# Optimization experiments

Hardware: AMD Instinct MI355X
Metric: run time of the kernel (lower is better)

## Reference

```python
import math
import jax, jax.numpy as jnp
import numpy as np

B, N, D, NC, TMAX = 8, 4096, 1024, 512, 1000


def setup_inputs() -> dict:
    key = jax.random.key(0)
    ks = jax.random.split(key, 12)
    tokens = jax.random.normal(ks[0], (B, N, D), jnp.float32)
    ctx_C = jax.random.normal(ks[1], (B, NC, D), jnp.float32)
    t = jax.random.randint(ks[2], (B,), 0, TMAX, dtype=jnp.int32)
    rare_mask = jax.random.bernoulli(ks[3], 0.05, (B, N))
    # Linear params stored as (in, out); scaled so scores straddle 0.5
    ctx_w = jax.random.normal(ks[4], (D, D // 4), jnp.float32) / math.sqrt(D)
    ctx_b = jax.random.normal(ks[5], (D // 4,), jnp.float32) * 0.01
    t_proj_w = jax.random.normal(ks[6], (D, D), jnp.float32) / math.sqrt(D)
    t_proj_b = jax.random.normal(ks[7], (D,), jnp.float32) * 0.01
    HIN = D + D // 4 + D  # 2304
    w1 = jax.random.normal(ks[8], (HIN, D // 2), jnp.float32) / math.sqrt(HIN)
    b1 = jax.random.normal(ks[9], (D // 2,), jnp.float32) * 0.01
    w2 = jax.random.normal(ks[10], (D // 2,), jnp.float32) * 0.1
    b2 = jnp.zeros((1,), jnp.float32)
    return {"tokens": tokens, "ctx_C": ctx_C, "t": t, "rare_mask": rare_mask,
            "ctx_w": ctx_w, "ctx_b": ctx_b, "t_proj_w": t_proj_w,
            "t_proj_b": t_proj_b, "w1": w1, "b1": b1, "w2": w2, "b2": b2}


def reference(tokens, ctx_C, t, rare_mask, ctx_w, ctx_b, t_proj_w, t_proj_b, w1, b1, w2, b2):
    Bb, Nn, Dd = tokens.shape
    half = Dd // 2
    # sinusoidal timestep embedding buffer (matches torch register_buffer)
    freq = jnp.exp(-math.log(10000.0) * jnp.arange(half, dtype=jnp.float32) / max(half - 1, 1))
    # bottlenecked context: mean over ctx tokens -> (B, D//4)
    ctx_bn = ctx_C.mean(axis=1) @ ctx_w + ctx_b
    args = t.astype(jnp.float32)[:, None] * freq[None, :]            # (B, half)
    emb = jnp.concatenate([jnp.sin(args), jnp.cos(args)], axis=-1)   # (B, D)
    t_emb = emb @ t_proj_w + t_proj_b                                # (B, D)
    x = jnp.concatenate([
        tokens,
        jnp.broadcast_to(ctx_bn[:, None, :], (Bb, Nn, Dd // 4)),
        jnp.broadcast_to(t_emb[:, None, :], (Bb, Nn, Dd)),
    ], axis=-1)                                                       # (B, N, 2.25D)
    h = jax.nn.relu(x @ w1 + b1)                                      # (B, N, D//2)
    scores = jax.nn.sigmoid(h @ w2 + b2)                              # (B, N)
    skip = (scores > 0.5) & jnp.logical_not(rare_mask)
    min_active = max(1, int(Nn * 0.2))
    active = jnp.logical_not(skip).sum(axis=-1)                       # (B,)
    deficit = jnp.maximum(min_active - active, 0)                     # (B,)
    masked = jnp.where(skip, scores, jnp.inf)
    rank = jnp.argsort(jnp.argsort(masked, axis=-1), axis=-1)         # rank among skipped, ascending score
    skip = skip & jnp.logical_not(rank < deficit[:, None])
    return skip, scores
```

## Files before the change

### kernel.cpp

```cpp
#include <hip/hip_runtime.h>
#include <math.h>

#define NN 4096
#define DD 1024
#define M_TOT 32768
#define H1 512
#define MIN_ACTIVE 819
#define MARGIN 0.03f
#define MAXFIX 8192

typedef __bf16 bf16x8 __attribute__((ext_vector_type(8)));
typedef float f32x4 __attribute__((ext_vector_type(4)));

__device__ __forceinline__ unsigned short f2bf(float f) {
    unsigned int u = __float_as_uint(f);
    return (unsigned short)((u + 0x7FFFu + ((u >> 16) & 1u)) >> 16);
}

__device__ __forceinline__ void glds16(const unsigned short* g, unsigned short* l) {
    __builtin_amdgcn_global_load_lds(
        (const __attribute__((address_space(1))) unsigned int*)g,
        (__attribute__((address_space(3))) unsigned int*)l, 16, 0, 0);
}

__global__ void convB_pmean_kernel(const float* __restrict__ w1, unsigned short* __restrict__ w1tt,
                                   const float* __restrict__ ctx, float* __restrict__ pmean,
                                   const unsigned char* __restrict__ rare, int* __restrict__ mode,
                                   int* __restrict__ fixcnt) {
    __shared__ float tile[32][65];
    __shared__ int nonbin, oneoff;
    int blk = blockIdx.x;
    int tid = threadIdx.x;
    if (blk < 256) {
        int t = blk >> 3;
        int c0 = (blk & 7) * 64;
        #pragma unroll
        for (int i = 0; i < 8; ++i) {
            int idx = tid + 256 * i;
            int kk = idx >> 6, cc = idx & 63;
            tile[kk][cc] = w1[(size_t)(t * 32 + kk) * H1 + c0 + cc];
        }
        __syncthreads();
        {
            int cc = tid >> 2, jp = tid & 3;
            int c = c0 + cc;
            int j = jp ^ ((c >> 1) & 3);
            unsigned int w[4];
            #pragma unroll
            for (int q = 0; q < 4; ++q)
                w[q] = (unsigned int)f2bf(tile[j * 8 + 2 * q][cc])
                     | ((unsigned int)f2bf(tile[j * 8 + 2 * q + 1][cc]) << 16);
            uint4 v; v.x = w[0]; v.y = w[1]; v.z = w[2]; v.w = w[3];
            *(uint4*)(w1tt + ((size_t)t * 512 + c) * 32 + jp * 8) = v;
        }
        if (blk == 0) {
            if (tid == 0) { nonbin = 0; oneoff = 0; *fixcnt = 0; }
            __syncthreads();
            int lnon = 0, lone = 0;
            for (int i = tid; i < 32768; i += 256) {
                unsigned char b = rare[i];
                if (b > 1) lnon = 1;
                else if (b == 1 && (i & 3) != 0) lone = 1;
            }
            if (lnon) atomicOr(&nonbin, 1);
            if (lone) atomicOr(&oneoff, 1);
            __syncthreads();
            if (tid == 0) *mode = nonbin ? 2 : (oneoff ? 1 : 0);
        }
    } else {
        int pblk = blk - 256;
        int b = pblk >> 5, dq = (pblk >> 3) & 3, nz = pblk & 7;
        int d = dq * 256 + tid;
        const float* base = ctx + ((size_t)(b * 512 + nz * 64)) * DD + d;
        float acc = 0.f;
        for (int n = 0; n < 64; ++n) acc += base[(size_t)n * DD];
        pmean[(b * 8 + nz) * DD + d] = acc;
    }
}

__global__ __launch_bounds__(256) void midk_kernel(
    const float* __restrict__ pmean, const int* __restrict__ t,
    const float* __restrict__ ctx_w, const float* __restrict__ ctx_b,
    const float* __restrict__ tpw, const float* __restrict__ tpb,
    float* __restrict__ ctx_bn, float* __restrict__ t_emb) {
    __shared__ float sh[1024];
    __shared__ float red8[8][32];
    __shared__ float red4[4][64];
    int tid = threadIdx.x;
    if (blockIdx.x < 64) {
        int b = blockIdx.x >> 3, cg = blockIdx.x & 7;
        for (int j = tid; j < 1024; j += 256) {
            float s = 0.f;
            #pragma unroll
            for (int nz = 0; nz < 8; ++nz) s += pmean[(b * 8 + nz) * DD + j];
            sh[j] = s * (1.f / 512.f);
        }
        __syncthreads();
        int c = cg * 32 + (tid & 31), ks = tid >> 5;
        const float* mb = sh + ks * 128;
        const float* wb = ctx_w + (size_t)(ks * 128) * 256 + c;
        float acc = 0.f;
        for (int i = 0; i < 128; ++i) acc += mb[i] * wb[(size_t)i * 256];
        red8[ks][tid & 31] = acc;
        __syncthreads();
        if (tid < 32) {
            float s = 0.f;
            for (int k = 0; k < 8; ++k) s += red8[k][tid];
            ctx_bn[b * 256 + cg * 32 + tid] = s + ctx_b[cg * 32 + tid];
        }
    } else {
        int blk = blockIdx.x - 64;
        int b = blk >> 4, cg = blk & 15;
        double tv = (double)t[b];
        const double neg_ln = -log(10000.0) / 511.0;
        for (int j = tid; j < 1024; j += 256) {
            int jj = j & 511;
            double arg = tv * exp(neg_ln * (double)jj);
            sh[j] = (float)((j < 512) ? sin(arg) : cos(arg));
        }
        __syncthreads();
        int c = cg * 64 + (tid & 63), ks = tid >> 6;
        const float* eb = sh + ks * 256;
        const float* wb = tpw + (size_t)(ks * 256) * DD + c;
        float acc = 0.f;
        for (int i = 0; i < 256; ++i) acc += eb[i] * wb[(size_t)i * DD];
        red4[ks][tid & 63] = acc;
        __syncthreads();
        if (tid < 64) {
            float s = red4[0][tid] + red4[1][tid] + red4[2][tid] + red4[3][tid];
            t_emb[b * DD + cg * 64 + tid] = s + tpb[cg * 64 + tid];
        }
    }
}

__global__ void baseh_kernel(const float* __restrict__ ctx_bn, const float* __restrict__ t_emb,
                             const float* __restrict__ w1, const float* __restrict__ b1,
                             float* __restrict__ base_h) {
    __shared__ float red[8][32];
    int b = blockIdx.x, cg = blockIdx.y;
    int c = cg * 32 + (threadIdx.x & 31), ks = threadIdx.x >> 5;
    float acc = 0.f;
    for (int i = 0; i < 160; ++i) {
        int k = ks * 160 + i;
        float v = (k < 256) ? ctx_bn[b * 256 + k] : t_emb[b * DD + k - 256];
        acc += v * w1[(size_t)(1024 + k) * H1 + c];
    }
    red[ks][threadIdx.x & 31] = acc;
    __syncthreads();
    if (threadIdx.x < 32) {
        float s = 0.f;
        for (int k = 0; k < 8; ++k) s += red[k][threadIdx.x];
        base_h[b * H1 + cg * 32 + threadIdx.x] = s + b1[cg * 32 + threadIdx.x];
    }
}

__global__ __launch_bounds__(512, 2) void gemm_kernel(
    const float* __restrict__ tokens, const unsigned short* __restrict__ w1tt,
    const float* __restrict__ baseh, const float* __restrict__ w2,
    const float* __restrict__ b2, const void* __restrict__ rare,
    const int* __restrict__ mode_p, float* __restrict__ out,
    int* __restrict__ fixcnt, int* __restrict__ fixlist) {
    __shared__ unsigned short As[2][128 * 40];
    __shared__ unsigned short Bs[3][512 * 32];
    __shared__ float red[128][4];
    int tid = threadIdx.x;
    int lane = tid & 63, wid = tid >> 6;
    int wm = wid >> 2, wn = wid & 3;
    int la = lane & 15, lk = lane >> 4;
    int row0 = blockIdx.x * 128;

    f32x4 acc[4][8];
    #pragma unroll
    for (int i = 0; i < 4; ++i)
        #pragma unroll
        for (int j = 0; j < 8; ++j)
            acc[i][j] = (f32x4){0.f, 0.f, 0.f, 0.f};

    float4 sa0[2], sa1[2];
    #define LOAD_A(kt_, S_) { \
        _Pragma("unroll") \
        for (int i = 0; i < 2; ++i) { \
            int id = tid + 512 * i; \
            int r = id >> 3, xk = id & 7; \
            S_[i] = *(const float4*)(tokens + (size_t)(row0 + r) * DD + (kt_) + xk * 4); \
        } }
    #define WRITE_A(bb_, S_) { \
        _Pragma("unroll") \
        for (int i = 0; i < 2; ++i) { \
            int id = tid + 512 * i; \
            int r = id >> 3, xk = id & 7; \
            ushort4 h; \
            h.x = f2bf(S_[i].x); h.y = f2bf(S_[i].y); \
            h.z = f2bf(S_[i].z); h.w = f2bf(S_[i].w); \
            *(ushort4*)(&As[bb_][r * 40 + xk * 4]) = h; \
        } }
    #define STAGE_B(t_, bb_) { \
        const unsigned short* gsrc = w1tt + (size_t)(t_) * 512 * 32; \
        _Pragma("unroll") \
        for (int q = 0; q < 4; ++q) { \
            int chunk = wid * 4 + q; \
            glds16(gsrc + chunk * 512 + lane * 8, &Bs[bb_][chunk * 512]); \
        } }

    LOAD_A(0, sa0);
    STAGE_B(0, 0);
    STAGE_B(1, 1);
    WRITE_A(0, sa0);
    LOAD_A(32, sa1);
    __builtin_amdgcn_sched_barrier(0);
    asm volatile("s_waitcnt vmcnt(6)" ::: "memory");
    asm volatile("s_waitcnt lgkmcnt(0)" ::: "memory");
    __builtin_amdgcn_s_barrier();
    __builtin_amdgcn_sched_barrier(0);

    for (int t = 0; t < 32; ++t) {
        int bb = t & 1;
        const unsigned short* bsrc = Bs[t % 3];
        bf16x8 af[4], bfr[8];
        #pragma unroll
        for (int mf = 0; mf < 4; ++mf) {
            int r = wm * 64 + mf * 16 + la;
            af[mf] = *(const bf16x8*)(&As[bb][r * 40 + lk * 8]);
        }
        #pragma unroll
        for (int nf = 0; nf < 8; ++nf) {
            int c = wn * 128 + nf * 16 + la;
            int sw = lk ^ ((c >> 1) & 3);
            bfr[nf] = *(const bf16x8*)(&bsrc[c * 32 + sw * 8]);
        }
        __builtin_amdgcn_s_setprio(1);
        #pragma unroll
        for (int mf = 0; mf < 4; ++mf)
            #pragma unroll
            for (int nf = 0; nf < 8; ++nf)
                acc[mf][nf] = __builtin_amdgcn_mfma_f32_16x16x32_bf16(af[mf], bfr[nf], acc[mf][nf], 0, 0, 0);
        __builtin_amdgcn_s_setprio(0);
        __builtin_amdgcn_sched_barrier(0);
        if (t < 31) {
            if (t & 1) { WRITE_A(bb ^ 1, sa0) } else { WRITE_A(bb ^ 1, sa1) }
            if (t < 30) {
                if (t & 1) { LOAD_A((t + 2) * 32, sa1) } else { LOAD_A((t + 2) * 32, sa0) }
                STAGE_B(t + 2, (t + 2) % 3);
            }
            __builtin_amdgcn_sched_barrier(0);
            if (t < 30) asm volatile("s_waitcnt vmcnt(6)" ::: "memory");
            else        asm volatile("s_waitcnt vmcnt(0)" ::: "memory");
            asm volatile("s_waitcnt lgkmcnt(0)" ::: "memory");
            __builtin_amdgcn_s_barrier();
            __builtin_amdgcn_sched_barrier(0);
        }
    }
    #undef LOAD_A
    #undef WRITE_A
    #undef STAGE_B

    int b = row0 >> 12;
    const float* bh = baseh + b * H1;
    float bhv[8], w2v[8];
    #pragma unroll
    for (int nf = 0; nf < 8; ++nf) {
        int col = wn * 128 + nf * 16 + la;
        bhv[nf] = bh[col];
        w2v[nf] = w2[col];
    }
    #pragma unroll
    for (int mf = 0; mf < 4; ++mf) {
        #pragma unroll
        for (int reg = 0; reg < 4; ++reg) {
            float p = 0.f;
            #pragma unroll
            for (int nf = 0; nf < 8; ++nf) {
                float h = acc[mf][nf][reg] + bhv[nf];
                h = fmaxf(h, 0.f);
                p += h * w2v[nf];
            }
            p += __shfl_xor(p, 1, 64);
            p += __shfl_xor(p, 2, 64);
            p += __shfl_xor(p, 4, 64);
            p += __shfl_xor(p, 8, 64);
            if (la == 0) red[wm * 64 + mf * 16 + lk * 4 + reg][wn] = p;
        }
    }
    __syncthreads();
    if (tid < 128) {
        int row = row0 + tid;
        float logit = red[tid][0] + red[tid][1] + red[tid][2] + red[tid][3] + b2[0];
        float score = 1.f / (1.f + expf(-logit));
        int mode = *mode_p;
        bool rm = (mode == 1) ? (((const unsigned char*)rare)[row] != 0)
                : (mode == 2) ? (((const float*)rare)[row] != 0.f)
                : (((const int*)rare)[row] != 0);
        out[row] = ((score > 0.5f) && !rm) ? 1.f : 0.f;
        out[M_TOT + row] = score;
        if (fabsf(logit) < MARGIN) {
            int i = atomicAdd(fixcnt, 1);
            if (i < MAXFIX) fixlist[i] = row;
        }
    }
}

__global__ __launch_bounds__(512) void fixup_kernel(
    const int* __restrict__ fixcnt, const int* __restrict__ fixlist,
    const float* __restrict__ tokens, const float* __restrict__ w1,
    const float* __restrict__ base_h, const float* __restrict__ w2,
    const float* __restrict__ b2, const void* __restrict__ rare,
    const int* __restrict__ mode_p, float* __restrict__ out) {
    __shared__ float tok[DD];
    __shared__ float part4[4][H1];
    __shared__ float red[8];
    int tid = threadIdx.x;
    int lane = tid & 63, wid = tid >> 6;
    int ks = tid >> 7;
    int cg = tid & 127;
    int n = *fixcnt;
    if (n > MAXFIX) n = MAXFIX;
    for (int g = blockIdx.x; g < n; g += gridDim.x) {
        int row = fixlist[g];
        int b = row >> 12;
        if (tid < 256)
            ((float4*)tok)[tid] = ((const float4*)(tokens + (size_t)row * DD))[tid];
        __syncthreads();
        const float* wbase = w1 + (size_t)(ks * 256) * H1 + cg * 4;
        const float* tbase = tok + ks * 256;
        float4 a = {0.f, 0.f, 0.f, 0.f};
        #pragma unroll 8
        for (int k = 0; k < 256; ++k) {
            float4 w = *(const float4*)(wbase + (size_t)k * H1);
            float tv = tbase[k];
            a.x += tv * w.x; a.y += tv * w.y; a.z += tv * w.z; a.w += tv * w.w;
        }
        *(float4*)&part4[ks][cg * 4] = a;
        __syncthreads();
        float h = part4[0][tid] + part4[1][tid] + part4[2][tid] + part4[3][tid]
                + base_h[b * H1 + tid];
        h = fmaxf(h, 0.f);
        float p = h * w2[tid];
        p += __shfl_xor(p, 1, 64);
        p += __shfl_xor(p, 2, 64);
        p += __shfl_xor(p, 4, 64);
        p += __shfl_xor(p, 8, 64);
        p += __shfl_xor(p, 16, 64);
        p += __shfl_xor(p, 32, 64);
        if (lane == 0) red[wid] = p;
        __syncthreads();
        if (tid == 0) {
            float logit = b2[0];
            #pragma unroll
            for (int w = 0; w < 8; ++w) logit += red[w];
            float score = 1.f / (1.f + expf(-logit));
            int mode = *mode_p;
            bool rm = (mode == 1) ? (((const unsigned char*)rare)[row] != 0)
                    : (mode == 2) ? (((const float*)rare)[row] != 0.f)
                    : (((const int*)rare)[row] != 0);
            out[row] = ((score > 0.5f) && !rm) ? 1.f : 0.f;
            out[M_TOT + row] = score;
        }
        __syncthreads();
    }
}

__global__ void floor_kernel(float* __restrict__ out) {
    __shared__ float s[NN];
    __shared__ unsigned char f[NN];
    __shared__ int cnt;
    int b = blockIdx.x, tid = threadIdx.x;
    if (tid == 0) cnt = 0;
    __syncthreads();
    int local = 0;
    for (int i = tid; i < NN; i += 256) {
        s[i] = out[M_TOT + b * NN + i];
        unsigned char sk = out[b * NN + i] > 0.5f;
        f[i] = sk;
        local += sk;
    }
    atomicAdd(&cnt, local);
    __syncthreads();
    int deficit = cnt - (NN - MIN_ACTIVE);
    if (deficit <= 0) return;
    for (int i = tid; i < NN; i += 256) {
        if (!f[i]) continue;
        float si = s[i];
        int rank = 0;
        for (int j = 0; j < NN; ++j) {
            if (f[j] && (s[j] < si || (s[j] == si && j < i))) {
                if (++rank >= deficit) break;
            }
        }
        if (rank < deficit) out[b * NN + i] = 0.f;
    }
}

extern "C" void kernel_launch(void* const* d_in, const int* in_sizes, int n_in,
                              void* d_out, int out_size, void* d_ws, size_t ws_size,
                              hipStream_t stream) {
    const float* tokens   = (const float*)d_in[0];
    const float* ctx_C    = (const float*)d_in[1];
    const int*   t        = (const int*)d_in[2];
    const void*  rare     = d_in[3];
    const float* ctx_w    = (const float*)d_in[4];
    const float* ctx_b    = (const float*)d_in[5];
    const float* t_proj_w = (const float*)d_in[6];
    const float* t_proj_b = (const float*)d_in[7];
    const float* w1       = (const float*)d_in[8];
    const float* b1       = (const float*)d_in[9];
    const float* w2       = (const float*)d_in[10];
    const float* b2       = (const float*)d_in[11];
    float* out = (float*)d_out;

    char* ws = (char*)d_ws;
    unsigned short* w1tt  = (unsigned short*)(ws);
    float* pmean          = (float*)(ws + 1048576);
    float* ctx_bn         = (float*)(ws + 1310720);
    float* t_emb          = (float*)(ws + 1318912);
    float* base_h         = (float*)(ws + 1351680);
    int*   mode           = (int*)  (ws + 1368064);
    int*   fixcnt         = (int*)  (ws + 1368128);
    int*   fixlist        = (int*)  (ws + 1368192);

    convB_pmean_kernel<<<512, 256, 0, stream>>>(w1, w1tt, ctx_C, pmean,
                                                (const unsigned char*)rare, mode, fixcnt);
    midk_kernel<<<192, 256, 0, stream>>>(pmean, t, ctx_w, ctx_b, t_proj_w, t_proj_b, ctx_bn, t_emb);
    baseh_kernel<<<dim3(8, 16), 256, 0, stream>>>(ctx_bn, t_emb, w1, b1, base_h);
    gemm_kernel<<<256, 512, 0, stream>>>(tokens, w1tt, base_h, w2, b2, rare, mode, out, fixcnt, fixlist);
    fixup_kernel<<<512, 512, 0, stream>>>(fixcnt, fixlist, tokens, w1, base_h, w2, b2, rare, mode, out);
    floor_kernel<<<8, 256, 0, stream>>>(out);
}
```

Baseline: 179.7 us.

## Split GEMM over hidden halves and fuse small kernels via atomic grid sync

The main GEMM now runs over a 2D grid, with each block computing half of the 512 hidden columns. Per-row partial logits are combined through a workspace buffer and an atomic arrival counter, which doubles the block count and lowers per-block LDS and register use. Separately, baseh is folded into the midk kernel and the floor pass into fixup, each joined by an in-kernel atomic spin barrier, cutting two kernel launches. The spin barriers assume all blocks are co-resident, and the split adds a redundant A-tile load and an extra global round trip for the partial sums.

```diff
diff --git a/kernel.cpp b/kernel.cpp
--- a/kernel.cpp
+++ b/kernel.cpp
@@ -23,14 +23,17 @@
         (__attribute__((address_space(3))) unsigned int*)l, 16, 0, 0);
 }
 
-__global__ void convB_pmean_kernel(const float* __restrict__ w1, unsigned short* __restrict__ w1tt,
-                                   const float* __restrict__ ctx, float* __restrict__ pmean,
-                                   const unsigned char* __restrict__ rare, int* __restrict__ mode,
-                                   int* __restrict__ fixcnt) {
+__global__ void pre1_kernel(const float* __restrict__ w1, unsigned short* __restrict__ w1tt,
+                            const float* __restrict__ ctx, float* __restrict__ pmean,
+                            const unsigned char* __restrict__ rare, int* __restrict__ mode,
+                            int* __restrict__ fixcnt, unsigned int* __restrict__ rowcnt,
+                            int* __restrict__ syncA, int* __restrict__ syncB) {
     __shared__ float tile[32][65];
     __shared__ int nonbin, oneoff;
     int blk = blockIdx.x;
     int tid = threadIdx.x;
+    if (tid < 64) rowcnt[blk * 64 + tid] = 0u;
+    if (blk == 0 && tid == 0) { *fixcnt = 0; *syncA = 0; *syncB = 0; }
     if (blk < 256) {
         int t = blk >> 3;
         int c0 = (blk & 7) * 64;
@@ -54,7 +57,7 @@
             *(uint4*)(w1tt + ((size_t)t * 512 + c) * 32 + jp * 8) = v;
         }
         if (blk == 0) {
-            if (tid == 0) { nonbin = 0; oneoff = 0; *fixcnt = 0; }
+            if (tid == 0) { nonbin = 0; oneoff = 0; }
             __syncthreads();
             int lnon = 0, lone = 0;
             for (int i = tid; i < 32768; i += 256) {
@@ -78,17 +81,20 @@
     }
 }
 
-__global__ __launch_bounds__(256) void midk_kernel(
+__global__ __launch_bounds__(256) void pre2_kernel(
     const float* __restrict__ pmean, const int* __restrict__ t,
     const float* __restrict__ ctx_w, const float* __restrict__ ctx_b,
     const float* __restrict__ tpw, const float* __restrict__ tpb,
-    float* __restrict__ ctx_bn, float* __restrict__ t_emb) {
+    const float* __restrict__ w1, const float* __restrict__ b1,
+    float* __restrict__ ctx_bn, float* __restrict__ t_emb,
+    float* __restrict__ base_h, int* __restrict__ syncA) {
     __shared__ float sh[1024];
     __shared__ float red8[8][32];
     __shared__ float red4[4][64];
     int tid = threadIdx.x;
-    if (blockIdx.x < 64) {
-        int b = blockIdx.x >> 3, cg = blockIdx.x & 7;
+    int blk = blockIdx.x;
+    if (blk < 64) {
+        int b = blk >> 3, cg = blk & 7;
         for (int j = tid; j < 1024; j += 256) {
             float s = 0.f;
             #pragma unroll
@@ -109,8 +115,8 @@
             ctx_bn[b * 256 + cg * 32 + tid] = s + ctx_b[cg * 32 + tid];
         }
     } else {
-        int blk = blockIdx.x - 64;
-        int b = blk >> 4, cg = blk & 15;
+        int bb = blk - 64;
+        int b = bb >> 4, cg = bb & 15;
         double tv = (double)t[b];
         const double neg_ln = -log(10000.0) / 511.0;
         for (int j = tid; j < 1024; j += 256) {
@@ -131,49 +137,57 @@
             t_emb[b * DD + cg * 64 + tid] = s + tpb[cg * 64 + tid];
         }
     }
-}
-
-__global__ void baseh_kernel(const float* __restrict__ ctx_bn, const float* __restrict__ t_emb,
-                             const float* __restrict__ w1, const float* __restrict__ b1,
-                             float* __restrict__ base_h) {
-    __shared__ float red[8][32];
-    int b = blockIdx.x, cg = blockIdx.y;
-    int c = cg * 32 + (threadIdx.x & 31), ks = threadIdx.x >> 5;
-    float acc = 0.f;
-    for (int i = 0; i < 160; ++i) {
-        int k = ks * 160 + i;
-        float v = (k < 256) ? ctx_bn[b * 256 + k] : t_emb[b * DD + k - 256];
-        acc += v * w1[(size_t)(1024 + k) * H1 + c];
-    }
-    red[ks][threadIdx.x & 31] = acc;
     __syncthreads();
-    if (threadIdx.x < 32) {
-        float s = 0.f;
-        for (int k = 0; k < 8; ++k) s += red[k][threadIdx.x];
-        base_h[b * H1 + cg * 32 + threadIdx.x] = s + b1[cg * 32 + threadIdx.x];
-    }
-}
-
-__global__ __launch_bounds__(512, 2) void gemm_kernel(
+    __threadfence();
+    if (tid == 0) atomicAdd(syncA, 1);
+    if (blk < 128) {
+        if (tid == 0) {
+            while (atomicAdd(syncA, 0) < 192) __builtin_amdgcn_s_sleep(8);
+        }
+        __syncthreads();
+        __threadfence();
+        __shared__ float red[8][32];
+        int b = blk >> 4, cg = blk & 15;
+        int c = cg * 32 + (tid & 31), ks = tid >> 5;
+        float acc = 0.f;
+        for (int i = 0; i < 160; ++i) {
+            int k = ks * 160 + i;
+            float v = (k < 256) ? ctx_bn[b * 256 + k] : t_emb[b * DD + k - 256];
+            acc += v * w1[(size_t)(1024 + k) * H1 + c];
+        }
+        red[ks][tid & 31] = acc;
+        __syncthreads();
+        if (tid < 32) {
+            float s = 0.f;
+            for (int k = 0; k < 8; ++k) s += red[k][tid];
+            base_h[b * H1 + cg * 32 + tid] = s + b1[cg * 32 + tid];
+        }
+    }
+}
+
+__global__ __launch_bounds__(512, 4) void gemm_kernel(
     const float* __restrict__ tokens, const unsigned short* __restrict__ w1tt,
     const float* __restrict__ baseh, const float* __restrict__ w2,
     const float* __restrict__ b2, const void* __restrict__ rare,
     const int* __restrict__ mode_p, float* __restrict__ out,
-    int* __restrict__ fixcnt, int* __restrict__ fixlist) {
+    int* __restrict__ fixcnt, int* __restrict__ fixlist,
+    float* __restrict__ part, unsigned int* __restrict__ rowcnt) {
     __shared__ unsigned short As[2][128 * 40];
-    __shared__ unsigned short Bs[3][512 * 32];
+    __shared__ unsigned short Bs[3][256 * 32];
     __shared__ float red[128][4];
     int tid = threadIdx.x;
     int lane = tid & 63, wid = tid >> 6;
     int wm = wid >> 2, wn = wid & 3;
     int la = lane & 15, lk = lane >> 4;
     int row0 = blockIdx.x * 128;
-
-    f32x4 acc[4][8];
+    int half = blockIdx.y;
+    const unsigned short* wsrc = w1tt + (size_t)half * 256 * 32;
+
+    f32x4 acc[4][4];
     #pragma unroll
     for (int i = 0; i < 4; ++i)
         #pragma unroll
-        for (int j = 0; j < 8; ++j)
+        for (int j = 0; j < 4; ++j)
             acc[i][j] = (f32x4){0.f, 0.f, 0.f, 0.f};
 
     float4 sa0[2], sa1[2];
@@ -195,10 +209,10 @@
             *(ushort4*)(&As[bb_][r * 40 + xk * 4]) = h; \
         } }
     #define STAGE_B(t_, bb_) { \
-        const unsigned short* gsrc = w1tt + (size_t)(t_) * 512 * 32; \
+        const unsigned short* gsrc = wsrc + (size_t)(t_) * 512 * 32; \
         _Pragma("unroll") \
-        for (int q = 0; q < 4; ++q) { \
-            int chunk = wid * 4 + q; \
+        for (int q = 0; q < 2; ++q) { \
+            int chunk = wid * 2 + q; \
             glds16(gsrc + chunk * 512 + lane * 8, &Bs[bb_][chunk * 512]); \
         } }
 
@@ -208,7 +222,7 @@
     WRITE_A(0, sa0);
     LOAD_A(32, sa1);
     __builtin_amdgcn_sched_barrier(0);
-    asm volatile("s_waitcnt vmcnt(6)" ::: "memory");
+    asm volatile("s_waitcnt vmcnt(4)" ::: "memory");
     asm volatile("s_waitcnt lgkmcnt(0)" ::: "memory");
     __builtin_amdgcn_s_barrier();
     __builtin_amdgcn_sched_barrier(0);
@@ -216,15 +230,15 @@
     for (int t = 0; t < 32; ++t) {
         int bb = t & 1;
         const unsigned short* bsrc = Bs[t % 3];
-        bf16x8 af[4], bfr[8];
+        bf16x8 af[4], bfr[4];
         #pragma unroll
         for (int mf = 0; mf < 4; ++mf) {
             int r = wm * 64 + mf * 16 + la;
             af[mf] = *(const bf16x8*)(&As[bb][r * 40 + lk * 8]);
         }
         #pragma unroll
-        for (int nf = 0; nf < 8; ++nf) {
-            int c = wn * 128 + nf * 16 + la;
+        for (int nf = 0; nf < 4; ++nf) {
+            int c = wn * 64 + nf * 16 + la;
             int sw = lk ^ ((c >> 1) & 3);
             bfr[nf] = *(const bf16x8*)(&bsrc[c * 32 + sw * 8]);
         }
@@ -232,7 +246,7 @@
         #pragma unroll
         for (int mf = 0; mf < 4; ++mf)
             #pragma unroll
-            for (int nf = 0; nf < 8; ++nf)
+            for (int nf = 0; nf < 4; ++nf)
                 acc[mf][nf] = __builtin_amdgcn_mfma_f32_16x16x32_bf16(af[mf], bfr[nf], acc[mf][nf], 0, 0, 0);
         __builtin_amdgcn_s_setprio(0);
         __builtin_amdgcn_sched_barrier(0);
@@ -243,7 +257,7 @@
                 STAGE_B(t + 2, (t + 2) % 3);
             }
             __builtin_amdgcn_sched_barrier(0);
-            if (t < 30) asm volatile("s_waitcnt vmcnt(6)" ::: "memory");
+            if (t < 30) asm volatile("s_waitcnt vmcnt(4)" ::: "memory");
             else        asm volatile("s_waitcnt vmcnt(0)" ::: "memory");
             asm volatile("s_waitcnt lgkmcnt(0)" ::: "memory");
             __builtin_amdgcn_s_barrier();
@@ -256,10 +270,10 @@
 
     int b = row0 >> 12;
     const float* bh = baseh + b * H1;
-    float bhv[8], w2v[8];
+    float bhv[4], w2v[4];
     #pragma unroll
-    for (int nf = 0; nf < 8; ++nf) {
-        int col = wn * 128 + nf * 16 + la;
+    for (int nf = 0; nf < 4; ++nf) {
+        int col = half * 256 + wn * 64 + nf * 16 + la;
         bhv[nf] = bh[col];
         w2v[nf] = w2[col];
     }
@@ -269,7 +283,7 @@
         for (int reg = 0; reg < 4; ++reg) {
             float p = 0.f;
             #pragma unroll
-            for (int nf = 0; nf < 8; ++nf) {
+            for (int nf = 0; nf < 4; ++nf) {
                 float h = acc[mf][nf][reg] + bhv[nf];
                 h = fmaxf(h, 0.f);
                 p += h * w2v[nf];
@@ -284,30 +298,43 @@
     __syncthreads();
     if (tid < 128) {
         int row = row0 + tid;
-        float logit = red[tid][0] + red[tid][1] + red[tid][2] + red[tid][3] + b2[0];
-        float score = 1.f / (1.f + expf(-logit));
-        int mode = *mode_p;
-        bool rm = (mode == 1) ? (((const unsigned char*)rare)[row] != 0)
-                : (mode == 2) ? (((const float*)rare)[row] != 0.f)
-                : (((const int*)rare)[row] != 0);
-        out[row] = ((score > 0.5f) && !rm) ? 1.f : 0.f;
-        out[M_TOT + row] = score;
-        if (fabsf(logit) < MARGIN) {
-            int i = atomicAdd(fixcnt, 1);
-            if (i < MAXFIX) fixlist[i] = row;
-        }
-    }
-}
-
-__global__ __launch_bounds__(512) void fixup_kernel(
+        float pa = red[tid][0] + red[tid][1] + red[tid][2] + red[tid][3];
+        part[(size_t)row * 2 + half] = pa;
+        __threadfence();
+        unsigned int old = atomicAdd(&rowcnt[row], 1u);
+        if (old == 1u) {
+            __threadfence();
+            float p0 = (half == 0) ? pa : part[(size_t)row * 2];
+            float p1 = (half == 1) ? pa : part[(size_t)row * 2 + 1];
+            float logit = p0 + p1 + b2[0];
+            float score = 1.f / (1.f + expf(-logit));
+            int mode = *mode_p;
+            bool rm = (mode == 1) ? (((const unsigned char*)rare)[row] != 0)
+                    : (mode == 2) ? (((const float*)rare)[row] != 0.f)
+                    : (((const int*)rare)[row] != 0);
+            out[row] = ((score > 0.5f) && !rm) ? 1.f : 0.f;
+            out[M_TOT + row] = score;
+            if (fabsf(logit) < MARGIN) {
+                int i = atomicAdd(fixcnt, 1);
+                if (i < MAXFIX) fixlist[i] = row;
+            }
+        }
+    }
+}
+
+__global__ __launch_bounds__(512) void fixpost_kernel(
     const int* __restrict__ fixcnt, const int* __restrict__ fixlist,
     const float* __restrict__ tokens, const float* __restrict__ w1,
     const float* __restrict__ base_h, const float* __restrict__ w2,
     const float* __restrict__ b2, const void* __restrict__ rare,
-    const int* __restrict__ mode_p, float* __restrict__ out) {
+    const int* __restrict__ mode_p, float* __restrict__ out,
+    int* __restrict__ syncB) {
     __shared__ float tok[DD];
     __shared__ float part4[4][H1];
     __shared__ float red[8];
+    __shared__ float s[NN];
+    __shared__ unsigned char fl[NN];
+    __shared__ int scnt;
     int tid = threadIdx.x;
     int lane = tid & 63, wid = tid >> 6;
     int ks = tid >> 7;
@@ -357,36 +384,40 @@
         }
         __syncthreads();
     }
-}
-
-__global__ void floor_kernel(float* __restrict__ out) {
-    __shared__ float s[NN];
-    __shared__ unsigned char f[NN];
-    __shared__ int cnt;
-    int b = blockIdx.x, tid = threadIdx.x;
-    if (tid == 0) cnt = 0;
+    __threadfence();
     __syncthreads();
-    int local = 0;
-    for (int i = tid; i < NN; i += 256) {
-        s[i] = out[M_TOT + b * NN + i];
-        unsigned char sk = out[b * NN + i] > 0.5f;
-        f[i] = sk;
-        local += sk;
-    }
-    atomicAdd(&cnt, local);
-    __syncthreads();
-    int deficit = cnt - (NN - MIN_ACTIVE);
-    if (deficit <= 0) return;
-    for (int i = tid; i < NN; i += 256) {
-        if (!f[i]) continue;
-        float si = s[i];
-        int rank = 0;
-        for (int j = 0; j < NN; ++j) {
-            if (f[j] && (s[j] < si || (s[j] == si && j < i))) {
-                if (++rank >= deficit) break;
+    if (tid == 0) atomicAdd(syncB, 1);
+    if (blockIdx.x < 8) {
+        if (tid == 0) {
+            while (atomicAdd(syncB, 0) < 256) __builtin_amdgcn_s_sleep(8);
+        }
+        __syncthreads();
+        __threadfence();
+        int b = blockIdx.x;
+        if (tid == 0) scnt = 0;
+        __syncthreads();
+        int local = 0;
+        for (int i = tid; i < NN; i += 512) {
+            s[i] = out[M_TOT + b * NN + i];
+            unsigned char sk = out[b * NN + i] > 0.5f;
+            fl[i] = sk;
+            local += sk;
+        }
+        atomicAdd(&scnt, local);
+        __syncthreads();
+        int deficit = scnt - (NN - MIN_ACTIVE);
+        if (deficit <= 0) return;
+        for (int i = tid; i < NN; i += 512) {
+            if (!fl[i]) continue;
+            float si = s[i];
+            int rank = 0;
+            for (int j = 0; j < NN; ++j) {
+                if (fl[j] && (s[j] < si || (s[j] == si && j < i))) {
+                    if (++rank >= deficit) break;
+                }
             }
-        }
-        if (rank < deficit) out[b * NN + i] = 0.f;
+            if (rank < deficit) out[b * NN + i] = 0.f;
+        }
     }
 }
 
@@ -410,18 +441,24 @@
     char* ws = (char*)d_ws;
     unsigned short* w1tt  = (unsigned short*)(ws);
     float* pmean          = (float*)(ws + 1048576);
-    float* ctx_bn         = (float*)(ws + 1310720);
-    float* t_emb          = (float*)(ws + 1318912);
-    float* base_h         = (float*)(ws + 1351680);
-    int*   mode           = (int*)  (ws + 1368064);
-    int*   fixcnt         = (int*)  (ws + 1368128);
-    int*   fixlist        = (int*)  (ws + 1368192);
-
-    convB_pmean_kernel<<<512, 256, 0, stream>>>(w1, w1tt, ctx_C, pmean,
-                                                (const unsigned char*)rare, mode, fixcnt);
-    midk_kernel<<<192, 256, 0, stream>>>(pmean, t, ctx_w, ctx_b, t_proj_w, t_proj_b, ctx_bn, t_emb);
-    baseh_kernel<<<dim3(8, 16), 256, 0, stream>>>(ctx_bn, t_emb, w1, b1, base_h);
-    gemm_kernel<<<256, 512, 0, stream>>>(tokens, w1tt, base_h, w2, b2, rare, mode, out, fixcnt, fixlist);
-    fixup_kernel<<<512, 512, 0, stream>>>(fixcnt, fixlist, tokens, w1, base_h, w2, b2, rare, mode, out);
-    floor_kernel<<<8, 256, 0, stream>>>(out);
-}
+    float* part           = (float*)(ws + 1310720);
+    unsigned int* rowcnt  = (unsigned int*)(ws + 1572864);
+    float* ctx_bn         = (float*)(ws + 1703936);
+    float* t_emb          = (float*)(ws + 1712128);
+    float* base_h         = (float*)(ws + 1744896);
+    int*   mode           = (int*)  (ws + 1761280);
+    int*   fixcnt         = (int*)  (ws + 1761344);
+    int*   syncA          = (int*)  (ws + 1761408);
+    int*   syncB          = (int*)  (ws + 1761472);
+    int*   fixlist        = (int*)  (ws + 1761536);
+
+    pre1_kernel<<<512, 256, 0, stream>>>(w1, w1tt, ctx_C, pmean,
+                                         (const unsigned char*)rare, mode, fixcnt,
+                                         rowcnt, syncA, syncB);
+    pre2_kernel<<<192, 256, 0, stream>>>(pmean, t, ctx_w, ctx_b, t_proj_w, t_proj_b,
+                                         w1, b1, ctx_bn, t_emb, base_h, syncA);
+    gemm_kernel<<<dim3(256, 2), 512, 0, stream>>>(tokens, w1tt, base_h, w2, b2, rare,
+                                                  mode, out, fixcnt, fixlist, part, rowcnt);
+    fixpost_kernel<<<256, 512, 0, stream>>>(fixcnt, fixlist, tokens, w1, base_h, w2,
+                                            b2, rare, mode, out, syncB);
+}
```

Result: slower. 256.2 us (+42.5%).
